# Kernel tuning notes

Measured on AMD Instinct MI355X. Metric: run time of the kernel, lower is better.

## Reference

```python
import jax, jax.numpy as jnp
import numpy as np

B, O, D = 4096, 256, 256  # batch, size_out (rules), size_in (features)


def setup_inputs() -> dict:
    key = jax.random.key(0)
    k1, k2, k3, k4, k5 = jax.random.split(key, 5)
    return {
        "x": jax.random.normal(k1, (B, D), dtype=jnp.float32),
        "scales": jax.random.normal(k2, (O, D), dtype=jnp.float32),
        # strict upper triangle holds the packed rot vectors (original inits them to zeros;
        # small values keep the quadratic form well conditioned)
        "rots": jax.random.normal(k3, (O, D, D), dtype=jnp.float32) * 0.02,
        "centroids": jax.random.normal(k4, (O, D, 1), dtype=jnp.float32),
        "b": jax.random.uniform(k5, (O,), dtype=jnp.float32, minval=0.5, maxval=1.5),
    }


def reference(x, scales, rots, centroids, b):
    # Build symmetric transform A[o] = diag(scales[o]) + triu(rots[o],1) + triu(rots[o],1)^T
    # (equivalent to the loop of diag_embed(r_i, i+1) + mirrored lower diagonal).
    upper = jnp.triu(rots, 1)                                   # [O,D,D]
    A = upper + jnp.swapaxes(upper, -1, -2)
    A = A + jnp.eye(D, dtype=scales.dtype) * scales[:, None, :]  # diag_embed(scales)
    # Augmented affine map: mul[o,i,b'] = A[o] @ x[b'] + centroid[o,i]; const row dropped
    # since only the first size_in rows feed the norm.
    y = jnp.einsum('bj,oij->boi', x, A) + centroids[..., 0][None, :, :]  # [B,O,D]
    rx = jnp.sqrt(jnp.sum(y * y, axis=-1))                      # L2 norm over D -> [B,O]
    return 1.0 / (1.0 + rx ** (2.0 * b))                        # bell membership [B,O]
```

## Files before the change

### kernel.cpp

```cpp
#include <hip/hip_runtime.h>
#include <cstdint>
#include <cmath>

#define Bn 4096
#define Dn 256
#define On 256

typedef __bf16 v8bf __attribute__((ext_vector_type(8)));
typedef float  v4f  __attribute__((ext_vector_type(4)));
typedef unsigned short us8 __attribute__((ext_vector_type(8)));

__device__ __forceinline__ unsigned short f2bf(float f) {
    unsigned int u = __builtin_bit_cast(unsigned int, f);
    unsigned int r = (u + 0x7fffu + ((u >> 16) & 1u)) >> 16;
    return (unsigned short)r;
}

__device__ __forceinline__ void gl_lds16(const void* g, void* l) {
    __builtin_amdgcn_global_load_lds(
        (const __attribute__((address_space(1))) void*)(uintptr_t)g,
        (__attribute__((address_space(3))) void*)(uintptr_t)l, 16, 0, 0);
}

__global__ __launch_bounds__(256) void build_A(
    const float* __restrict__ scales, const float* __restrict__ rots,
    unsigned short* __restrict__ Ab) {
    static const int TI[10] = {0, 0, 0, 0, 1, 1, 1, 2, 2, 3};
    static const int TJ[10] = {0, 1, 2, 3, 1, 2, 3, 2, 3, 3};
    const int o  = blockIdx.y;
    const int ti = TI[blockIdx.x], tj = TJ[blockIdx.x];
    const int tid = threadIdx.x;
    const int r = tid >> 3;
    const int c = (tid & 7) * 8;

    __shared__ float t[64][65];
    const float* src = rots + (size_t)o * Dn * Dn + (size_t)(ti * 64) * Dn + tj * 64;
    unsigned short* dstU = Ab + (size_t)o * Dn * Dn + (size_t)(ti * 64) * Dn + tj * 64;
    unsigned short* dstL = Ab + (size_t)o * Dn * Dn + (size_t)(tj * 64) * Dn + ti * 64;

    float f[2][8];
#pragma unroll
    for (int s = 0; s < 2; ++s) {
        const int rr = s * 32 + r;
        const float4 v0 = *(const float4*)(src + rr * Dn + c);
        const float4 v1 = *(const float4*)(src + rr * Dn + c + 4);
        f[s][0] = v0.x; f[s][1] = v0.y; f[s][2] = v0.z; f[s][3] = v0.w;
        f[s][4] = v1.x; f[s][5] = v1.y; f[s][6] = v1.z; f[s][7] = v1.w;
#pragma unroll
        for (int q = 0; q < 8; ++q) t[rr][c + q] = f[s][q];
    }
    __syncthreads();

    if (ti != tj) {
#pragma unroll
        for (int s = 0; s < 2; ++s) {
            const int rr = s * 32 + r;
            us8 u;
#pragma unroll
            for (int q = 0; q < 8; ++q) u[q] = f2bf(f[s][q]);
            *(us8*)(dstU + rr * Dn + c) = u;
        }
#pragma unroll
        for (int s = 0; s < 2; ++s) {
            const int rr = s * 32 + r;
            us8 u;
#pragma unroll
            for (int q = 0; q < 8; ++q) u[q] = f2bf(t[c + q][rr]);
            *(us8*)(dstL + rr * Dn + c) = u;
        }
    } else {
#pragma unroll
        for (int s = 0; s < 2; ++s) {
            const int rr = s * 32 + r;
            us8 u;
#pragma unroll
            for (int q = 0; q < 8; ++q) {
                const int jj = c + q;
                const float v = (rr < jj) ? t[rr][jj]
                              : ((rr > jj) ? t[jj][rr]
                                           : scales[o * Dn + ti * 64 + rr]);
                u[q] = f2bf(v);
            }
            *(us8*)(dstU + rr * Dn + c) = u;
        }
    }
}

__global__ __launch_bounds__(256) void cvt_x(const float* __restrict__ x,
                                             unsigned short* __restrict__ xb) {
    const int i = (blockIdx.x * 256 + threadIdx.x) * 4;
    const float4 v = *(const float4*)(x + i);
    ushort4 u;
    u.x = f2bf(v.x); u.y = f2bf(v.y); u.z = f2bf(v.z); u.w = f2bf(v.w);
    *(ushort4*)(xb + i) = u;
}

__global__ __launch_bounds__(256, 2) void fuzzy_main(
    const unsigned short* __restrict__ Ab, const unsigned short* __restrict__ xb,
    const float* __restrict__ cent, const float* __restrict__ bvals,
    float* __restrict__ obase, int sb, int so) {
    constexpr int BK = 64;
    __shared__ __align__(16) unsigned short Xs[128 * BK];
    __shared__ __align__(16) unsigned short As[256 * BK];
    __shared__ float ssbuf[4][128];
    __shared__ float centL[Dn];

    const int tid  = threadIdx.x;
    const int lane = tid & 63;
    const int wv   = tid >> 6;
    const int b0   = blockIdx.x * 128;
    const int o    = blockIdx.y;

    centL[tid] = cent[o * Dn + tid];

    const int frow = lane & 15, quad = lane >> 4;
    const int lr = lane >> 3, ls = lane & 7;
    const int ksw = (ls ^ lr) * 8;
    const size_t Aoff = (size_t)o * Dn * Dn;

    v4f acc[4][8];
#pragma unroll
    for (int mi = 0; mi < 4; ++mi)
#pragma unroll
        for (int ni = 0; ni < 8; ++ni)
            acc[mi][ni] = v4f{0.f, 0.f, 0.f, 0.f};

    for (int k0 = 0; k0 < Dn; k0 += BK) {
#pragma unroll
        for (int q = 0; q < 4; ++q) {
            const int row = (wv * 4 + q) * 8 + lr;
            gl_lds16(xb + (size_t)(b0 + row) * Dn + k0 + ksw,
                     &Xs[row * BK + ls * 8]);
        }
#pragma unroll
        for (int q = 0; q < 8; ++q) {
            const int row = (wv * 8 + q) * 8 + lr;
            gl_lds16(Ab + Aoff + (size_t)row * Dn + k0 + ksw,
                     &As[row * BK + ls * 8]);
        }
        __syncthreads();
#pragma unroll
        for (int ks = 0; ks < 2; ++ks) {
            const int slot = (ks * 4 + quad) ^ (frow & 7);
            v8bf af[4], xf[8];
#pragma unroll
            for (int mi = 0; mi < 4; ++mi) {
                const int rr = wv * 64 + mi * 16 + frow;
                af[mi] = *(const v8bf*)&As[rr * BK + slot * 8];
            }
#pragma unroll
            for (int ni = 0; ni < 8; ++ni) {
                const int rr = ni * 16 + frow;
                xf[ni] = *(const v8bf*)&Xs[rr * BK + slot * 8];
            }
#pragma unroll
            for (int mi = 0; mi < 4; ++mi)
#pragma unroll
                for (int ni = 0; ni < 8; ++ni)
                    acc[mi][ni] = __builtin_amdgcn_mfma_f32_16x16x32_bf16(
                        af[mi], xf[ni], acc[mi][ni], 0, 0, 0);
        }
        __syncthreads();
    }

    float cv[4][4];
#pragma unroll
    for (int mi = 0; mi < 4; ++mi)
#pragma unroll
        for (int rg = 0; rg < 4; ++rg)
            cv[mi][rg] = centL[wv * 64 + mi * 16 + quad * 4 + rg];
#pragma unroll
    for (int ni = 0; ni < 8; ++ni) {
        float v = 0.f;
#pragma unroll
        for (int mi = 0; mi < 4; ++mi)
#pragma unroll
            for (int rg = 0; rg < 4; ++rg) {
                const float y = acc[mi][ni][rg] + cv[mi][rg];
                v += y * y;
            }
        v += __shfl_xor(v, 16);
        v += __shfl_xor(v, 32);
        if (lane < 16) ssbuf[wv][ni * 16 + lane] = v;
    }
    __syncthreads();
    if (tid < 128) {
        const float ssq = ssbuf[0][tid] + ssbuf[1][tid] + ssbuf[2][tid] + ssbuf[3][tid];
        obase[(size_t)(b0 + tid) * sb + (size_t)o * so] =
            1.0f / (1.0f + powf(ssq, bvals[o]));
    }
}

__global__ __launch_bounds__(256) void transp(const float* __restrict__ outT,
                                              float* __restrict__ out) {
    __shared__ float t[64][65];
    const int bb = blockIdx.x * 64;
    const int ob = blockIdx.y * 64;
    const int tid = threadIdx.x;
    const int r = tid >> 4;
    const int c = (tid & 15) * 4;
#pragma unroll
    for (int s = 0; s < 4; ++s) {
        const int rr = s * 16 + r;
        const float4 v = *(const float4*)(outT + (size_t)(ob + rr) * Bn + bb + c);
        t[rr][c] = v.x; t[rr][c + 1] = v.y; t[rr][c + 2] = v.z; t[rr][c + 3] = v.w;
    }
    __syncthreads();
#pragma unroll
    for (int s = 0; s < 4; ++s) {
        const int rr = s * 16 + r;
        float4 w;
        w.x = t[c][rr]; w.y = t[c + 1][rr]; w.z = t[c + 2][rr]; w.w = t[c + 3][rr];
        *(float4*)(out + (size_t)(bb + rr) * On + ob + c) = w;
    }
}

__global__ void fallback_kernel(const float* __restrict__ x, const float* __restrict__ scales,
                                const float* __restrict__ rots, const float* __restrict__ cent,
                                const float* __restrict__ bvals, float* __restrict__ out) {
    const int b = blockIdx.x * blockDim.x + threadIdx.x;
    const int o = blockIdx.y;
    if (b >= Bn) return;
    const float* R  = rots + (size_t)o * Dn * Dn;
    const float* xv = x + (size_t)b * Dn;
    float ss = 0.f;
    for (int i = 0; i < Dn; ++i) {
        float a = cent[o * Dn + i];
        for (int j = 0; j < Dn; ++j) {
            const float w = (j > i) ? R[i * Dn + j]
                          : ((j < i) ? R[j * Dn + i] : scales[o * Dn + i]);
            a += w * xv[j];
        }
        ss += a * a;
    }
    out[(size_t)b * On + o] = 1.f / (1.f + powf(ss, bvals[o]));
}

extern "C" void kernel_launch(void* const* d_in, const int* in_sizes, int n_in,
                              void* d_out, int out_size, void* d_ws, size_t ws_size,
                              hipStream_t stream) {
    const float* x         = (const float*)d_in[0];
    const float* scales    = (const float*)d_in[1];
    const float* rots      = (const float*)d_in[2];
    const float* centroids = (const float*)d_in[3];
    const float* bvals     = (const float*)d_in[4];
    float* out = (float*)d_out;

    const size_t needA = (size_t)On * Dn * Dn * sizeof(unsigned short);
    const size_t needX = (size_t)Bn * Dn * sizeof(unsigned short);
    const size_t needT = (size_t)On * Bn * sizeof(float);

    if (ws_size >= needA + needX) {
        unsigned short* Ab = (unsigned short*)d_ws;
        unsigned short* xb = (unsigned short*)((char*)d_ws + needA);
        build_A<<<dim3(10, On), 256, 0, stream>>>(scales, rots, Ab);
        cvt_x<<<dim3((Bn * Dn) / 1024), 256, 0, stream>>>(x, xb);
        if (ws_size >= needA + needX + needT) {
            float* outT = (float*)((char*)d_ws + needA + needX);
            fuzzy_main<<<dim3(Bn / 128, On), 256, 0, stream>>>(Ab, xb, centroids, bvals,
                                                               outT, 1, Bn);
            transp<<<dim3(Bn / 64, On / 64), 256, 0, stream>>>(outT, out);
        } else {
            fuzzy_main<<<dim3(Bn / 128, On), 256, 0, stream>>>(Ab, xb, centroids, bvals,
                                                               out, On, 1);
        }
    } else {
        fallback_kernel<<<dim3(Bn / 256, On), 256, 0, stream>>>(x, scales, rots, centroids,
                                                                bvals, out);
    }
}
```

Measured before the change: 251.5 us.

## Switch main GEMM to 32x32x16 MFMA and merge prep kernels into one launch

The main kernel now uses 32x32x16 bf16 MFMA tiles (2x4 per wave) in place of 16x16x32 tiles (4x8). This needs fewer LDS fragment loads per MFMA and fewer instructions overall. The epilogue is remapped to the 32x32 accumulator layout and reads centroids directly from LDS. The A-matrix build and the x bf16 conversion are merged into a single prep launch, saving one kernel launch; each conversion block now handles four times as many elements.

```diff
diff --git a/kernel.cpp b/kernel.cpp
--- a/kernel.cpp
+++ b/kernel.cpp
@@ -7,7 +7,7 @@
 #define On 256
 
 typedef __bf16 v8bf __attribute__((ext_vector_type(8)));
-typedef float  v4f  __attribute__((ext_vector_type(4)));
+typedef float  v16f __attribute__((ext_vector_type(16)));
 typedef unsigned short us8 __attribute__((ext_vector_type(8)));
 
 __device__ __forceinline__ unsigned short f2bf(float f) {
@@ -22,14 +22,31 @@
         (__attribute__((address_space(3))) void*)(uintptr_t)l, 16, 0, 0);
 }
 
-__global__ __launch_bounds__(256) void build_A(
+__global__ __launch_bounds__(256) void prep(
     const float* __restrict__ scales, const float* __restrict__ rots,
-    unsigned short* __restrict__ Ab) {
+    const float* __restrict__ x, unsigned short* __restrict__ Ab,
+    unsigned short* __restrict__ xb) {
+    const int bid = blockIdx.x;
+    const int tid = threadIdx.x;
+
+    if (bid >= 2560) {
+        const int cb = bid - 2560;
+#pragma unroll
+        for (int s = 0; s < 4; ++s) {
+            const int i = cb * 4096 + s * 1024 + tid * 4;
+            const float4 v = *(const float4*)(x + i);
+            ushort4 u;
+            u.x = f2bf(v.x); u.y = f2bf(v.y); u.z = f2bf(v.z); u.w = f2bf(v.w);
+            *(ushort4*)(xb + i) = u;
+        }
+        return;
+    }
+
     static const int TI[10] = {0, 0, 0, 0, 1, 1, 1, 2, 2, 3};
     static const int TJ[10] = {0, 1, 2, 3, 1, 2, 3, 2, 3, 3};
-    const int o  = blockIdx.y;
-    const int ti = TI[blockIdx.x], tj = TJ[blockIdx.x];
-    const int tid = threadIdx.x;
+    const int o  = bid / 10;
+    const int p  = bid - o * 10;
+    const int ti = TI[p], tj = TJ[p];
     const int r = tid >> 3;
     const int c = (tid & 7) * 8;
 
@@ -84,15 +101,6 @@
             *(us8*)(dstU + rr * Dn + c) = u;
         }
     }
-}
-
-__global__ __launch_bounds__(256) void cvt_x(const float* __restrict__ x,
-                                             unsigned short* __restrict__ xb) {
-    const int i = (blockIdx.x * 256 + threadIdx.x) * 4;
-    const float4 v = *(const float4*)(x + i);
-    ushort4 u;
-    u.x = f2bf(v.x); u.y = f2bf(v.y); u.z = f2bf(v.z); u.w = f2bf(v.w);
-    *(ushort4*)(xb + i) = u;
 }
 
 __global__ __launch_bounds__(256, 2) void fuzzy_main(
@@ -113,17 +121,20 @@
 
     centL[tid] = cent[o * Dn + tid];
 
-    const int frow = lane & 15, quad = lane >> 4;
+    const int m32  = lane & 31;
+    const int half = lane >> 5;
     const int lr = lane >> 3, ls = lane & 7;
     const int ksw = (ls ^ lr) * 8;
     const size_t Aoff = (size_t)o * Dn * Dn;
 
-    v4f acc[4][8];
-#pragma unroll
-    for (int mi = 0; mi < 4; ++mi)
-#pragma unroll
-        for (int ni = 0; ni < 8; ++ni)
-            acc[mi][ni] = v4f{0.f, 0.f, 0.f, 0.f};
+    v16f acc[2][4];
+#pragma unroll
+    for (int mi = 0; mi < 2; ++mi)
+#pragma unroll
+        for (int ni = 0; ni < 4; ++ni)
+#pragma unroll
+            for (int rg = 0; rg < 16; ++rg)
+                acc[mi][ni][rg] = 0.f;
 
     for (int k0 = 0; k0 < Dn; k0 += BK) {
 #pragma unroll
@@ -140,48 +151,44 @@
         }
         __syncthreads();
 #pragma unroll
-        for (int ks = 0; ks < 2; ++ks) {
-            const int slot = (ks * 4 + quad) ^ (frow & 7);
-            v8bf af[4], xf[8];
-#pragma unroll
-            for (int mi = 0; mi < 4; ++mi) {
-                const int rr = wv * 64 + mi * 16 + frow;
-                af[mi] = *(const v8bf*)&As[rr * BK + slot * 8];
-            }
-#pragma unroll
-            for (int ni = 0; ni < 8; ++ni) {
-                const int rr = ni * 16 + frow;
-                xf[ni] = *(const v8bf*)&Xs[rr * BK + slot * 8];
-            }
-#pragma unroll
-            for (int mi = 0; mi < 4; ++mi)
-#pragma unroll
-                for (int ni = 0; ni < 8; ++ni)
-                    acc[mi][ni] = __builtin_amdgcn_mfma_f32_16x16x32_bf16(
+        for (int t = 0; t < 4; ++t) {
+            const int slot = ((t * 2 + half) ^ ls) * 8;
+            v8bf af[2], xf[4];
+#pragma unroll
+            for (int mi = 0; mi < 2; ++mi) {
+                const int rr = wv * 64 + mi * 32 + m32;
+                af[mi] = *(const v8bf*)&As[rr * BK + slot];
+            }
+#pragma unroll
+            for (int ni = 0; ni < 4; ++ni) {
+                const int rr = ni * 32 + m32;
+                xf[ni] = *(const v8bf*)&Xs[rr * BK + slot];
+            }
+#pragma unroll
+            for (int mi = 0; mi < 2; ++mi)
+#pragma unroll
+                for (int ni = 0; ni < 4; ++ni)
+                    acc[mi][ni] = __builtin_amdgcn_mfma_f32_32x32x16_bf16(
                         af[mi], xf[ni], acc[mi][ni], 0, 0, 0);
         }
         __syncthreads();
     }
 
-    float cv[4][4];
-#pragma unroll
-    for (int mi = 0; mi < 4; ++mi)
-#pragma unroll
-        for (int rg = 0; rg < 4; ++rg)
-            cv[mi][rg] = centL[wv * 64 + mi * 16 + quad * 4 + rg];
-#pragma unroll
-    for (int ni = 0; ni < 8; ++ni) {
+#pragma unroll
+    for (int ni = 0; ni < 4; ++ni) {
         float v = 0.f;
 #pragma unroll
-        for (int mi = 0; mi < 4; ++mi)
-#pragma unroll
-            for (int rg = 0; rg < 4; ++rg) {
-                const float y = acc[mi][ni][rg] + cv[mi][rg];
+        for (int mi = 0; mi < 2; ++mi) {
+            const int ibase = wv * 64 + mi * 32 + half * 4;
+#pragma unroll
+            for (int rg = 0; rg < 16; ++rg) {
+                const int io = (rg & 3) + 8 * (rg >> 2);
+                const float y = acc[mi][ni][rg] + centL[ibase + io];
                 v += y * y;
             }
-        v += __shfl_xor(v, 16);
+        }
         v += __shfl_xor(v, 32);
-        if (lane < 16) ssbuf[wv][ni * 16 + lane] = v;
+        if (lane < 32) ssbuf[wv][ni * 32 + lane] = v;
     }
     __syncthreads();
     if (tid < 128) {
@@ -253,8 +260,7 @@
     if (ws_size >= needA + needX) {
         unsigned short* Ab = (unsigned short*)d_ws;
         unsigned short* xb = (unsigned short*)((char*)d_ws + needA);
-        build_A<<<dim3(10, On), 256, 0, stream>>>(scales, rots, Ab);
-        cvt_x<<<dim3((Bn * Dn) / 1024), 256, 0, stream>>>(x, xb);
+        prep<<<dim3(2816), 256, 0, stream>>>(scales, rots, x, Ab, xb);
         if (ws_size >= needA + needX + needT) {
             float* outT = (float*)((char*)d_ws + needA + needX);
             fuzzy_main<<<dim3(Bn / 128, On), 256, 0, stream>>>(Ab, xb, centroids, bvals,
```

Result: no change. 255.8 us (+1.7%).

## Pre-swizzle A into MFMA fragment layout, stream A from global, stage full X tile

Applied to the files above, without the earlier changes.

The prep kernel now writes the bf16 A matrices already arranged in MFMA fragment order, and it absorbs the x conversion into a single launch. The main kernel loads the whole 128x256 X tile into LDS once and reads A fragments straight from global memory into registers, double-buffered. This removes the per-K-step LDS staging of A and the barriers that went with it. It also remaps block indices so blocks sharing the same rule o are spread across XCDs/L2. LDS use grows to 64KB per block, which may reduce occupancy, and A reads now rely on the L2 cache.

```diff
diff --git a/kernel.cpp b/kernel.cpp
--- a/kernel.cpp
+++ b/kernel.cpp
@@ -22,101 +22,116 @@
         (__attribute__((address_space(3))) void*)(uintptr_t)l, 16, 0, 0);
 }
 
-__global__ __launch_bounds__(256) void build_A(
+__global__ __launch_bounds__(256) void prep(
     const float* __restrict__ scales, const float* __restrict__ rots,
-    unsigned short* __restrict__ Ab) {
+    const float* __restrict__ x, unsigned short* __restrict__ Ap,
+    unsigned short* __restrict__ xb) {
+    const int bid = blockIdx.x;
+    const int tid = threadIdx.x;
+
+    if (bid >= 2560) {
+        const int cb = bid - 2560;
+#pragma unroll
+        for (int s = 0; s < 4; ++s) {
+            const int i = cb * 4096 + s * 1024 + tid * 4;
+            const float4 v = *(const float4*)(x + i);
+            ushort4 u;
+            u.x = f2bf(v.x); u.y = f2bf(v.y); u.z = f2bf(v.z); u.w = f2bf(v.w);
+            *(ushort4*)(xb + i) = u;
+        }
+        return;
+    }
+
     static const int TI[10] = {0, 0, 0, 0, 1, 1, 1, 2, 2, 3};
     static const int TJ[10] = {0, 1, 2, 3, 1, 2, 3, 2, 3, 3};
-    const int o  = blockIdx.y;
-    const int ti = TI[blockIdx.x], tj = TJ[blockIdx.x];
-    const int tid = threadIdx.x;
-    const int r = tid >> 3;
-    const int c = (tid & 7) * 8;
-
-    __shared__ float t[64][65];
+    const int o  = bid / 10;
+    const int p  = bid - o * 10;
+    const int ti = TI[p], tj = TJ[p];
+
+    __shared__ float t[64][68];
     const float* src = rots + (size_t)o * Dn * Dn + (size_t)(ti * 64) * Dn + tj * 64;
-    unsigned short* dstU = Ab + (size_t)o * Dn * Dn + (size_t)(ti * 64) * Dn + tj * 64;
-    unsigned short* dstL = Ab + (size_t)o * Dn * Dn + (size_t)(tj * 64) * Dn + ti * 64;
-
-    float f[2][8];
-#pragma unroll
-    for (int s = 0; s < 2; ++s) {
-        const int rr = s * 32 + r;
-        const float4 v0 = *(const float4*)(src + rr * Dn + c);
-        const float4 v1 = *(const float4*)(src + rr * Dn + c + 4);
-        f[s][0] = v0.x; f[s][1] = v0.y; f[s][2] = v0.z; f[s][3] = v0.w;
-        f[s][4] = v1.x; f[s][5] = v1.y; f[s][6] = v1.z; f[s][7] = v1.w;
-#pragma unroll
-        for (int q = 0; q < 8; ++q) t[rr][c + q] = f[s][q];
-    }
-    __syncthreads();
+#pragma unroll
+    for (int s = 0; s < 4; ++s) {
+        const int idx = s * 256 + tid;
+        const int r = idx >> 4, c = (idx & 15) * 4;
+        const float4 v = *(const float4*)(src + r * Dn + c);
+        *(float4*)&t[r][c] = v;
+    }
+    __syncthreads();
+
+#pragma unroll
+    for (int it = 0; it < 2; ++it) {
+        const int slot = it * 256 + tid;
+        const int bk = slot >> 6, L = slot & 63;
+        const int quad = L >> 4, frow = L & 15;
+        const int sl = bk >> 1, kl = bk & 1;
+        const int r = sl * 16 + frow, c = kl * 32 + quad * 8;
+        float v[8];
+        if (ti == tj) {
+#pragma unroll
+            for (int q = 0; q < 8; ++q) {
+                const int cc = c + q;
+                v[q] = (r < cc) ? t[r][cc]
+                     : ((r > cc) ? t[cc][r] : scales[o * Dn + ti * 64 + r]);
+            }
+        } else {
+            const float4 a = *(const float4*)&t[r][c];
+            const float4 b = *(const float4*)&t[r][c + 4];
+            v[0] = a.x; v[1] = a.y; v[2] = a.z; v[3] = a.w;
+            v[4] = b.x; v[5] = b.y; v[6] = b.z; v[7] = b.w;
+        }
+        us8 u;
+#pragma unroll
+        for (int q = 0; q < 8; ++q) u[q] = f2bf(v[q]);
+        const size_t off = ((size_t)((o * 16 + ti * 4 + sl) * 8 + tj * 2 + kl)) * 512 + L * 8;
+        *(us8*)(Ap + off) = u;
+    }
 
     if (ti != tj) {
 #pragma unroll
-        for (int s = 0; s < 2; ++s) {
-            const int rr = s * 32 + r;
+        for (int it = 0; it < 2; ++it) {
+            const int slot = it * 256 + tid;
+            const int bk = slot >> 6, L = slot & 63;
+            const int quad = L >> 4, frow = L & 15;
+            const int sl = bk >> 1, kl = bk & 1;
+            const int r = sl * 16 + frow, c = kl * 32 + quad * 8;
             us8 u;
 #pragma unroll
-            for (int q = 0; q < 8; ++q) u[q] = f2bf(f[s][q]);
-            *(us8*)(dstU + rr * Dn + c) = u;
-        }
-#pragma unroll
-        for (int s = 0; s < 2; ++s) {
-            const int rr = s * 32 + r;
-            us8 u;
-#pragma unroll
-            for (int q = 0; q < 8; ++q) u[q] = f2bf(t[c + q][rr]);
-            *(us8*)(dstL + rr * Dn + c) = u;
-        }
-    } else {
-#pragma unroll
-        for (int s = 0; s < 2; ++s) {
-            const int rr = s * 32 + r;
-            us8 u;
-#pragma unroll
-            for (int q = 0; q < 8; ++q) {
-                const int jj = c + q;
-                const float v = (rr < jj) ? t[rr][jj]
-                              : ((rr > jj) ? t[jj][rr]
-                                           : scales[o * Dn + ti * 64 + rr]);
-                u[q] = f2bf(v);
-            }
-            *(us8*)(dstU + rr * Dn + c) = u;
-        }
-    }
-}
-
-__global__ __launch_bounds__(256) void cvt_x(const float* __restrict__ x,
-                                             unsigned short* __restrict__ xb) {
-    const int i = (blockIdx.x * 256 + threadIdx.x) * 4;
-    const float4 v = *(const float4*)(x + i);
-    ushort4 u;
-    u.x = f2bf(v.x); u.y = f2bf(v.y); u.z = f2bf(v.z); u.w = f2bf(v.w);
-    *(ushort4*)(xb + i) = u;
+            for (int q = 0; q < 8; ++q) u[q] = f2bf(t[c + q][r]);
+            const size_t off = ((size_t)((o * 16 + tj * 4 + sl) * 8 + ti * 2 + kl)) * 512 + L * 8;
+            *(us8*)(Ap + off) = u;
+        }
+    }
 }
 
 __global__ __launch_bounds__(256, 2) void fuzzy_main(
-    const unsigned short* __restrict__ Ab, const unsigned short* __restrict__ xb,
+    const unsigned short* __restrict__ Ap, const unsigned short* __restrict__ xb,
     const float* __restrict__ cent, const float* __restrict__ bvals,
     float* __restrict__ obase, int sb, int so) {
-    constexpr int BK = 64;
-    __shared__ __align__(16) unsigned short Xs[128 * BK];
-    __shared__ __align__(16) unsigned short As[256 * BK];
+    __shared__ __align__(16) unsigned short Xs[128 * 256];
     __shared__ float ssbuf[4][128];
     __shared__ float centL[Dn];
 
     const int tid  = threadIdx.x;
     const int lane = tid & 63;
     const int wv   = tid >> 6;
-    const int b0   = blockIdx.x * 128;
-    const int o    = blockIdx.y;
+    const int Lb = blockIdx.x;
+    const int o  = (Lb & 7) * 32 + (Lb >> 8);
+    const int b0 = ((Lb >> 3) & 31) * 128;
 
     centL[tid] = cent[o * Dn + tid];
 
-    const int frow = lane & 15, quad = lane >> 4;
-    const int lr = lane >> 3, ls = lane & 7;
-    const int ksw = (ls ^ lr) * 8;
-    const size_t Aoff = (size_t)o * Dn * Dn;
+#pragma unroll
+    for (int q = 0; q < 16; ++q) {
+        const int R   = wv * 16 + q;
+        const int row = 2 * R + (lane >> 5);
+        const int g   = (lane & 31) ^ (row & 7);
+        gl_lds16(xb + (size_t)(b0 + row) * Dn + g * 8, &Xs[R * 512 + lane * 8]);
+    }
+    __syncthreads();
+
+    const int frow = lane & 15, quad = lane >> 4, f3 = lane & 7;
+    const unsigned short* Aw = Ap + (size_t)(o * 16 + wv * 4) * 4096;
 
     v4f acc[4][8];
 #pragma unroll
@@ -125,42 +140,30 @@
         for (int ni = 0; ni < 8; ++ni)
             acc[mi][ni] = v4f{0.f, 0.f, 0.f, 0.f};
 
-    for (int k0 = 0; k0 < Dn; k0 += BK) {
-#pragma unroll
-        for (int q = 0; q < 4; ++q) {
-            const int row = (wv * 4 + q) * 8 + lr;
-            gl_lds16(xb + (size_t)(b0 + row) * Dn + k0 + ksw,
-                     &Xs[row * BK + ls * 8]);
-        }
-#pragma unroll
-        for (int q = 0; q < 8; ++q) {
-            const int row = (wv * 8 + q) * 8 + lr;
-            gl_lds16(Ab + Aoff + (size_t)row * Dn + k0 + ksw,
-                     &As[row * BK + ls * 8]);
-        }
-        __syncthreads();
-#pragma unroll
-        for (int ks = 0; ks < 2; ++ks) {
-            const int slot = (ks * 4 + quad) ^ (frow & 7);
-            v8bf af[4], xf[8];
-#pragma unroll
-            for (int mi = 0; mi < 4; ++mi) {
-                const int rr = wv * 64 + mi * 16 + frow;
-                af[mi] = *(const v8bf*)&As[rr * BK + slot * 8];
-            }
-#pragma unroll
-            for (int ni = 0; ni < 8; ++ni) {
-                const int rr = ni * 16 + frow;
-                xf[ni] = *(const v8bf*)&Xs[rr * BK + slot * 8];
-            }
+    v8bf af[2][4];
+#pragma unroll
+    for (int mi = 0; mi < 4; ++mi)
+        af[0][mi] = *(const v8bf*)(Aw + (size_t)mi * 8 * 512 + lane * 8);
+
+#pragma unroll
+    for (int t = 0; t < 8; ++t) {
+        const int cur = t & 1, nxt = cur ^ 1;
+        if (t < 7) {
 #pragma unroll
             for (int mi = 0; mi < 4; ++mi)
-#pragma unroll
-                for (int ni = 0; ni < 8; ++ni)
-                    acc[mi][ni] = __builtin_amdgcn_mfma_f32_16x16x32_bf16(
-                        af[mi], xf[ni], acc[mi][ni], 0, 0, 0);
-        }
-        __syncthreads();
+                af[nxt][mi] = *(const v8bf*)(Aw + (size_t)(mi * 8 + t + 1) * 512 + lane * 8);
+        }
+        v8bf xf[8];
+        const int sl = (t * 4 + quad) ^ f3;
+#pragma unroll
+        for (int ni = 0; ni < 8; ++ni)
+            xf[ni] = *(const v8bf*)&Xs[(ni * 16 + frow) * 256 + sl * 8];
+#pragma unroll
+        for (int mi = 0; mi < 4; ++mi)
+#pragma unroll
+            for (int ni = 0; ni < 8; ++ni)
+                acc[mi][ni] = __builtin_amdgcn_mfma_f32_16x16x32_bf16(
+                    af[cur][mi], xf[ni], acc[mi][ni], 0, 0, 0);
     }
 
     float cv[4][4];
@@ -251,18 +254,17 @@
     const size_t needT = (size_t)On * Bn * sizeof(float);
 
     if (ws_size >= needA + needX) {
-        unsigned short* Ab = (unsigned short*)d_ws;
+        unsigned short* Ap = (unsigned short*)d_ws;
         unsigned short* xb = (unsigned short*)((char*)d_ws + needA);
-        build_A<<<dim3(10, On), 256, 0, stream>>>(scales, rots, Ab);
-        cvt_x<<<dim3((Bn * Dn) / 1024), 256, 0, stream>>>(x, xb);
+        prep<<<dim3(2816), 256, 0, stream>>>(scales, rots, x, Ap, xb);
         if (ws_size >= needA + needX + needT) {
             float* outT = (float*)((char*)d_ws + needA + needX);
-            fuzzy_main<<<dim3(Bn / 128, On), 256, 0, stream>>>(Ab, xb, centroids, bvals,
-                                                               outT, 1, Bn);
+            fuzzy_main<<<dim3(8192), 256, 0, stream>>>(Ap, xb, centroids, bvals,
+                                                       outT, 1, Bn);
             transp<<<dim3(Bn / 64, On / 64), 256, 0, stream>>>(outT, out);
         } else {
-            fuzzy_main<<<dim3(Bn / 128, On), 256, 0, stream>>>(Ab, xb, centroids, bvals,
-                                                               out, On, 1);
+            fuzzy_main<<<dim3(8192), 256, 0, stream>>>(Ap, xb, centroids, bvals,
+                                                       out, On, 1);
         }
     } else {
         fallback_kernel<<<dim3(Bn / 256, On), 256, 0, stream>>>(x, scales, rots, centroids,
```

New measurement: 249.4 us. Within noise of the previous version (-0.8%).
